# Optimization experiments

Measured on AMD Instinct MI355X. Metric: run time of the kernel, lower is better.

## Reference

```python
import jax, jax.numpy as jnp
import numpy as np

B, N_N, N_A, D = 1024, 96, 96, 512


def _normalize(x):
    return x / jnp.linalg.norm(x, axis=-1, keepdims=True)


def setup_inputs() -> dict:
    key = jax.random.key(0)
    ks = jax.random.split(key, 8)
    img_embs = _normalize(jax.random.normal(ks[0], (B, D), jnp.float32))
    normal_text_embs = _normalize(jax.random.normal(ks[1], (N_N, D), jnp.float32))
    abnormal_text_embs = _normalize(jax.random.normal(ks[2], (N_A, D), jnp.float32))
    logit_scale = jnp.full((1,), np.log(100.0), jnp.float32)  # CLIP temperature
    W1 = jax.random.normal(ks[3], (2 * D, D), jnp.float32) / np.sqrt(2 * D)
    b1 = jnp.zeros((D,), jnp.float32)
    W2 = jax.random.normal(ks[4], (D, D // 2), jnp.float32) / np.sqrt(D)
    b2 = jnp.zeros((D // 2,), jnp.float32)
    W3 = jax.random.normal(ks[5], (D // 2, D // 4), jnp.float32) / np.sqrt(D // 2)
    b3 = jnp.zeros((D // 4,), jnp.float32)
    return {"img_embs": img_embs, "normal_text_embs": normal_text_embs,
            "abnormal_text_embs": abnormal_text_embs, "logit_scale": logit_scale,
            "W1": W1, "b1": b1, "W2": W2, "b2": b2, "W3": W3, "b3": b3}


def _mlp(x, W1, b1, W2, b2, W3, b3):
    h = jax.nn.relu(x @ W1 + b1)
    h = jax.nn.relu(h @ W2 + b2)
    return h @ W3 + b3


def _branch(img_embs, text_embs, scale, W1, b1, W2, b2, W3, b3):
    # sims: [B, N]; softmax weights then exp-scaled text embeddings
    sims = (img_embs @ text_embs.T) * scale
    w = jax.nn.softmax(sims, axis=-1)
    scaled_text = text_embs[None, :, :] * jnp.exp(w)[:, :, None]      # [B, N, D]
    rep_img = jnp.broadcast_to(img_embs[:, None, :], scaled_text.shape)  # [B, N, D]
    x = jnp.concatenate([rep_img, scaled_text], axis=-1)              # [B, N, 2D]
    h = _mlp(x, W1, b1, W2, b2, W3, b3)                               # [B, N, D//4]
    return h.mean(axis=1)                                             # [B, D//4]


def reference(img_embs, normal_text_embs, abnormal_text_embs, logit_scale,
              W1, b1, W2, b2, W3, b3):
    scale = jnp.exp(logit_scale[0])
    h_n = _branch(img_embs, normal_text_embs, scale, W1, b1, W2, b2, W3, b3)
    h_a = _branch(img_embs, abnormal_text_embs, scale, W1, b1, W2, b2, W3, b3)
    return (h_n, h_a)
```

## Files before the change

### kernel.cpp

```cpp
#include <hip/hip_runtime.h>
#include <hip/hip_bf16.h>


typedef __attribute__((ext_vector_type(8))) short short8;
typedef __attribute__((ext_vector_type(4))) float floatx4;
typedef __attribute__((ext_vector_type(2))) float float2v;
typedef __attribute__((ext_vector_type(4))) unsigned int uint4v;

__device__ __forceinline__ unsigned short f2bf(float x) {
    unsigned int u = __float_as_uint(x);
    u += 0x7fffu + ((u >> 16) & 1u);
    return (unsigned short)(u >> 16);
}

template <bool BF16OUT>
__device__ __forceinline__ void gemm32(
    const float* __restrict__ A0, const float* __restrict__ A1, int rows0,
    const float* __restrict__ Bm, float* __restrict__ Cf,
    unsigned short* __restrict__ Cb, int mt, int nt, float* sAT, int t) {
    int r0 = mt * 32, c0 = nt * 64;
    int rg = t >> 4, cg = t & 15;
    int lrow = t >> 3, k4 = (t & 7) * 4;
    int gr = r0 + lrow;
    const float* Ap = (gr < rows0) ? (A0 + gr * 512) : (A1 + (gr - rows0) * 512);
    float acc[2][4];
#pragma unroll
    for (int r = 0; r < 2; r++)
#pragma unroll
        for (int c = 0; c < 4; c++) acc[r][c] = 0.f;
    const float* Bp = Bm + c0 + cg * 4;
    for (int k0 = 0; k0 < 512; k0 += 32) {
        __syncthreads();
        float4 av = *(const float4*)(Ap + k0 + k4);
        sAT[(k4 + 0) * 34 + lrow] = av.x;
        sAT[(k4 + 1) * 34 + lrow] = av.y;
        sAT[(k4 + 2) * 34 + lrow] = av.z;
        sAT[(k4 + 3) * 34 + lrow] = av.w;
        __syncthreads();
#pragma unroll 8
        for (int kk = 0; kk < 32; kk++) {
            float a0 = sAT[kk * 34 + rg * 2];
            float a1 = sAT[kk * 34 + rg * 2 + 1];
            float4 bv = *(const float4*)(Bp + (k0 + kk) * 512);
            acc[0][0] = fmaf(a0, bv.x, acc[0][0]); acc[0][1] = fmaf(a0, bv.y, acc[0][1]);
            acc[0][2] = fmaf(a0, bv.z, acc[0][2]); acc[0][3] = fmaf(a0, bv.w, acc[0][3]);
            acc[1][0] = fmaf(a1, bv.x, acc[1][0]); acc[1][1] = fmaf(a1, bv.y, acc[1][1]);
            acc[1][2] = fmaf(a1, bv.z, acc[1][2]); acc[1][3] = fmaf(a1, bv.w, acc[1][3]);
        }
    }
    int rr = r0 + rg * 2, cc = c0 + cg * 4;
#pragma unroll
    for (int r = 0; r < 2; r++) {
        if (BF16OUT) {
            unsigned long long pk =
                (unsigned long long)f2bf(acc[r][0]) | ((unsigned long long)f2bf(acc[r][1]) << 16) |
                ((unsigned long long)f2bf(acc[r][2]) << 32) | ((unsigned long long)f2bf(acc[r][3]) << 48);
            *(unsigned long long*)(Cb + (rr + r) * 512 + cc) = pk;
        } else {
            *(float4*)(Cf + (rr + r) * 512 + cc) = make_float4(acc[r][0], acc[r][1], acc[r][2], acc[r][3]);
        }
    }
}

__global__ __launch_bounds__(256) void prep_kernel(
    const float* __restrict__ img, const float* __restrict__ tn,
    const float* __restrict__ ta, const float* __restrict__ ls,
    const float* __restrict__ W1, const float* __restrict__ W2,
    float* __restrict__ e_ws, float* __restrict__ U_ws,
    unsigned short* __restrict__ Tb, unsigned short* __restrict__ W2Tf) {
    __shared__ __align__(16) float smem[8704];
    int idx = blockIdx.x;
    int t = threadIdx.x;

    if (idx < 256) {
        int bi0 = idx * 4;
        float* sImg = smem;
        float* sS   = smem + 2064;
        float* sMx  = smem + 2832;
        float* sSum = smem + 2840;
#pragma unroll
        for (int p = 0; p < 2; p++) {
            int i4 = t + 256 * p;
            int i = i4 >> 7, k4 = (i4 & 127) * 4;
            float4 v = *(const float4*)(img + (bi0 + i) * 512 + k4);
            sImg[i * 516 + k4 + 0] = v.x; sImg[i * 516 + k4 + 1] = v.y;
            sImg[i * 516 + k4 + 2] = v.z; sImg[i * 516 + k4 + 3] = v.w;
        }
        __syncthreads();
        float scale = __expf(ls[0]);
        int i = t & 3, n0 = (t >> 2) * 3;
        const float* txp[3];
#pragma unroll
        for (int r = 0; r < 3; r++) {
            int n = n0 + r;
            txp[r] = (n < 96) ? (tn + n * 512) : (ta + (n - 96) * 512);
        }
        float d0 = 0.f, d1 = 0.f, d2 = 0.f;
        const float* ib = &sImg[i * 516];
#pragma unroll 4
        for (int k4 = 0; k4 < 512; k4 += 4) {
            float4 iv = *(const float4*)(ib + k4);
            float4 a = *(const float4*)(txp[0] + k4);
            float4 b = *(const float4*)(txp[1] + k4);
            float4 c = *(const float4*)(txp[2] + k4);
            d0 += iv.x * a.x + iv.y * a.y + iv.z * a.z + iv.w * a.w;
            d1 += iv.x * b.x + iv.y * b.y + iv.z * b.z + iv.w * b.w;
            d2 += iv.x * c.x + iv.y * c.y + iv.z * c.z + iv.w * c.w;
        }
        sS[i * 192 + n0 + 0] = d0 * scale;
        sS[i * 192 + n0 + 1] = d1 * scale;
        sS[i * 192 + n0 + 2] = d2 * scale;
        __syncthreads();
        if (t < 8) {
            int ii = t >> 1, brx = t & 1;
            const float* base = &sS[ii * 192 + brx * 96];
            float m = -1e30f;
            for (int n = 0; n < 96; n++) m = fmaxf(m, base[n]);
            float s = 0.f;
            for (int n = 0; n < 96; n++) s += __expf(base[n] - m);
            sMx[t] = m; sSum[t] = s;
        }
        __syncthreads();
#pragma unroll
        for (int p = 0; p < 3; p++) {
            int j = t + 256 * p;
            int ii = j & 3, n = j >> 2;
            int brx = (n >= 96) ? 1 : 0;
            int nn = n - brx * 96;
            float w = __expf(sS[ii * 192 + n] - sMx[ii * 2 + brx]) / sSum[ii * 2 + brx];
            e_ws[(brx * 1024 + bi0 + ii) * 96 + nn] = __expf(w);
        }
    } else if (idx < 512) {
        int i2 = idx - 256;
        gemm32<false>(img, img, 1 << 20, W1, U_ws, nullptr, i2 >> 3, i2 & 7, smem, t);
    } else if (idx < 560) {
        int i2 = idx - 512;
        gemm32<true>(tn, ta, 96, W1 + 512 * 512, nullptr, Tb, i2 >> 3, i2 & 7, smem, t);
    } else {
        int kt = idx - 560;
        int k0 = kt * 32;
        float* sWT = smem;
        int kr = t >> 3, n0 = (t & 7) * 32;
#pragma unroll
        for (int c = 0; c < 8; c++) {
            float4 v = *(const float4*)(W2 + (k0 + kr) * 256 + n0 + c * 4);
            sWT[(n0 + c * 4 + 0) * 33 + kr] = v.x;
            sWT[(n0 + c * 4 + 1) * 33 + kr] = v.y;
            sWT[(n0 + c * 4 + 2) * 33 + kr] = v.z;
            sWT[(n0 + c * 4 + 3) * 33 + kr] = v.w;
        }
        __syncthreads();
        int lane = t & 63;
        int kl = (lane >> 4) * 8;
#pragma unroll
        for (int it = 0; it < 4; it++) {
            int nt = it * 4 + (t >> 6);
            int n = nt * 16 + (lane & 15);
            uint4v u;
#pragma unroll
            for (int c = 0; c < 4; c++) {
                unsigned short lo = f2bf(sWT[n * 33 + kl + 2 * c]);
                unsigned short hi = f2bf(sWT[n * 33 + kl + 2 * c + 1]);
                u[c] = (unsigned int)lo | ((unsigned int)hi << 16);
            }
            *(uint4v*)(W2Tf + (((kt * 16 + nt) * 64) + lane) * 8) = u;
        }
    }
}

__device__ __forceinline__ uint4v stage8(float ev, short8 tv, const float2v* u2) {
    uint4v tp; __builtin_memcpy(&tp, &tv, 16);
    float2v e2 = {ev, ev};
    const float2v z2 = {0.f, 0.f};
    uint4v pk;
#pragma unroll
    for (int jj = 0; jj < 4; jj++) {
        float2v t2;
        t2.x = __uint_as_float(tp[jj] << 16);
        t2.y = __uint_as_float(tp[jj] & 0xffff0000u);
        float2v f = __builtin_elementwise_fma(e2, t2, u2[jj]);
        f = __builtin_elementwise_max(f, z2);
        __hip_bfloat162 h2 = __float22bfloat162_rn(make_float2(f.x, f.y));
        unsigned int bits; __builtin_memcpy(&bits, &h2, 4);
        pk[jj] = bits;
    }
    return pk;
}

__global__ __launch_bounds__(256, 3) void branch_mlp9(
    const float* __restrict__ U, const unsigned short* __restrict__ Tb,
    const float* __restrict__ e_all, const unsigned short* __restrict__ W2Tf,
    const float* __restrict__ b1, const float* __restrict__ b2,
    const float* __restrict__ W3, const float* __restrict__ b3,
    float* __restrict__ out) {
    int b = blockIdx.x, br = blockIdx.y;
    const unsigned short* T = Tb + br * (96 * 512);

    __shared__ float sUb[512];
    __shared__ float sE[96];
    __shared__ __align__(16) unsigned short sH[2][96 * 64];
    __shared__ float sM2[256];
    __shared__ float sPart[256];

    int t = threadIdx.x;
    sUb[t] = U[b * 512 + t] + b1[t];
    sUb[t + 256] = U[b * 512 + t + 256] + b1[t + 256];
    if (t < 96) sE[t] = e_all[(br * 1024 + b) * 96 + t];

    const int wave = t >> 6, lane = t & 63;
    const int frow = lane & 15, fkq = (lane >> 4) * 8;
    const int f7 = frow & 7;
    const int srow = t >> 3;
    const int skc = (t & 7) * 8;
    const int sw = skc ^ ((srow & 7) * 8);
    const int ka0 = (((fkq >> 3) ^ f7) << 3);
    const int ka1 = (((4 + (fkq >> 3)) ^ f7) << 3);

    const floatx4 fz = {0.f, 0.f, 0.f, 0.f};
    floatx4 acc[6][4];
#pragma unroll
    for (int mt = 0; mt < 6; mt++)
#pragma unroll
        for (int j = 0; j < 4; j++) acc[mt][j] = fz;

    short8 tv[3];
#pragma unroll
    for (int i2 = 0; i2 < 3; i2++)
        tv[i2] = *(const short8*)(T + (srow + 32 * i2) * 512 + skc);
    const unsigned short* Wf = W2Tf + (wave * 4 * 64 + lane) * 8;

    __syncthreads();

    float ev[3];
#pragma unroll
    for (int i2 = 0; i2 < 3; i2++) ev[i2] = sE[srow + 32 * i2];

    {
        float2v u2[4];
#pragma unroll
        for (int jj = 0; jj < 4; jj++) u2[jj] = *(const float2v*)(&sUb[skc + 2 * jj]);
#pragma unroll
        for (int i2 = 0; i2 < 3; i2++)
            *(uint4v*)(&sH[0][(srow + 32 * i2) * 64 + sw]) = stage8(ev[i2], tv[i2], u2);
    }

#pragma unroll
    for (int s = 0; s < 8; s++) {
        int k0 = s * 64;
        unsigned short* sHb = sH[s & 1];
        __syncthreads();

        short8 b0f[4], b1f[4];
#pragma unroll
        for (int j = 0; j < 4; j++)
            b0f[j] = *(const short8*)(Wf + ((2 * s) * 16 + j) * (64 * 8));
#pragma unroll
        for (int j = 0; j < 4; j++)
            b1f[j] = *(const short8*)(Wf + ((2 * s + 1) * 16 + j) * (64 * 8));
        if (s < 7) {
#pragma unroll
            for (int i2 = 0; i2 < 3; i2++)
                tv[i2] = *(const short8*)(T + (srow + 32 * i2) * 512 + k0 + 64 + skc);
        }

#pragma unroll
        for (int mt = 0; mt < 6; mt++) {
            short8 afr = *(const short8*)(&sHb[(mt * 16 + frow) * 64 + ka0]);
#pragma unroll
            for (int j = 0; j < 4; j++)
                acc[mt][j] = __builtin_amdgcn_mfma_f32_16x16x32_bf16(afr, b0f[j], acc[mt][j], 0, 0, 0);
        }
#pragma unroll
        for (int mt = 0; mt < 6; mt++) {
            short8 afr = *(const short8*)(&sHb[(mt * 16 + frow) * 64 + ka1]);
#pragma unroll
            for (int j = 0; j < 4; j++)
                acc[mt][j] = __builtin_amdgcn_mfma_f32_16x16x32_bf16(afr, b1f[j], acc[mt][j], 0, 0, 0);
        }

        if (s < 7) {
            unsigned short* sHn = sH[(s + 1) & 1];
            float2v u2[4];
#pragma unroll
            for (int jj = 0; jj < 4; jj++) u2[jj] = *(const float2v*)(&sUb[k0 + 64 + skc + 2 * jj]);
#pragma unroll
            for (int i2 = 0; i2 < 3; i2++)
                *(uint4v*)(&sHn[(srow + 32 * i2) * 64 + sw]) = stage8(ev[i2], tv[i2], u2);
        }
    }

#pragma unroll
    for (int j = 0; j < 4; j++) {
        int col = wave * 64 + j * 16 + frow;
        float bb = b2[col];
        float s = 0.f;
#pragma unroll
        for (int mt = 0; mt < 6; mt++)
#pragma unroll
            for (int r = 0; r < 4; r++)
                s += fmaxf(acc[mt][j][r] + bb, 0.f);
        s += __shfl_xor(s, 16);
        s += __shfl_xor(s, 32);
        if (lane < 16) sM2[col] = s * (1.0f / 96.0f);
    }
    __syncthreads();

    int col = t & 127, ks2 = t >> 7;
    const float* w3p = W3 + (ks2 * 128) * 128 + col;
    const float* mp = sM2 + ks2 * 128;
    float o = 0.f;
#pragma unroll 8
    for (int k = 0; k < 128; k++) o = fmaf(mp[k], w3p[k * 128], o);
    sPart[t] = o;
    __syncthreads();
    if (t < 128) out[(br * 1024 + b) * 128 + t] = sPart[t] + sPart[t + 128] + b3[t];
}

extern "C" void kernel_launch(void* const* d_in, const int* in_sizes, int n_in,
                              void* d_out, int out_size, void* d_ws, size_t ws_size,
                              hipStream_t stream) {
    const float* img = (const float*)d_in[0];
    const float* tn  = (const float*)d_in[1];
    const float* ta  = (const float*)d_in[2];
    const float* ls  = (const float*)d_in[3];
    const float* W1  = (const float*)d_in[4];
    const float* b1  = (const float*)d_in[5];
    const float* W2  = (const float*)d_in[6];
    const float* b2  = (const float*)d_in[7];
    const float* W3  = (const float*)d_in[8];
    const float* b3  = (const float*)d_in[9];
    float* out = (float*)d_out;
    float* ws  = (float*)d_ws;

    float* e_ws = ws;
    float* U_ws = ws + 196608;
    unsigned short* Tb   = (unsigned short*)(ws + 720896);
    unsigned short* W2Tf = (unsigned short*)(ws + 770048);

    prep_kernel<<<576, 256, 0, stream>>>(img, tn, ta, ls, W1, W2, e_ws, U_ws, Tb, W2Tf);
    branch_mlp9<<<dim3(1024, 2), 256, 0, stream>>>(U_ws, Tb, e_ws, W2Tf, b1, b2, W3, b3, out);
}
```

Before: 177.5 us.

## Split branch MLP block across 8 waves to halve per-wave accumulators

Doubles the branch_mlp block to 512 threads, so each of 8 waves computes 32 output columns instead of 64, which halves the accumulator and B-fragment registers per wave. The staging work for the 96 rows is redistributed: the first 256 threads stage two rows and the rest stage one. The final W3 reduction is split four ways. The goal is more resident waves per CU to hide latency. In exchange, each A fragment is reused across fewer MFMAs, LDS reads per MFMA rise, and the staging load across threads is uneven.

New measurement: 177.5 us. About the same (+0.0%).

```diff
diff --git a/kernel.cpp b/kernel.cpp
--- a/kernel.cpp
+++ b/kernel.cpp
@@ -187,7 +187,7 @@
     return pk;
 }
 
-__global__ __launch_bounds__(256, 3) void branch_mlp9(
+__global__ __launch_bounds__(512, 4) void branch_mlp11(
     const float* __restrict__ U, const unsigned short* __restrict__ Tb,
     const float* __restrict__ e_all, const unsigned short* __restrict__ W2Tf,
     const float* __restrict__ b1, const float* __restrict__ b2,
@@ -200,48 +200,45 @@
     __shared__ float sE[96];
     __shared__ __align__(16) unsigned short sH[2][96 * 64];
     __shared__ float sM2[256];
-    __shared__ float sPart[256];
+    __shared__ float sPart[512];
 
     int t = threadIdx.x;
     sUb[t] = U[b * 512 + t] + b1[t];
-    sUb[t + 256] = U[b * 512 + t + 256] + b1[t + 256];
     if (t < 96) sE[t] = e_all[(br * 1024 + b) * 96 + t];
 
     const int wave = t >> 6, lane = t & 63;
     const int frow = lane & 15, fkq = (lane >> 4) * 8;
     const int f7 = frow & 7;
-    const int srow = t >> 3;
+    const bool two = (t < 256);
+    const int srowA = two ? (t >> 3) : (64 + ((t - 256) >> 3));
+    const int srowB = two ? (srowA + 32) : srowA;
     const int skc = (t & 7) * 8;
-    const int sw = skc ^ ((srow & 7) * 8);
+    const int sw = skc ^ ((srowA & 7) * 8);
     const int ka0 = (((fkq >> 3) ^ f7) << 3);
     const int ka1 = (((4 + (fkq >> 3)) ^ f7) << 3);
 
     const floatx4 fz = {0.f, 0.f, 0.f, 0.f};
-    floatx4 acc[6][4];
-#pragma unroll
-    for (int mt = 0; mt < 6; mt++)
-#pragma unroll
-        for (int j = 0; j < 4; j++) acc[mt][j] = fz;
-
-    short8 tv[3];
-#pragma unroll
-    for (int i2 = 0; i2 < 3; i2++)
-        tv[i2] = *(const short8*)(T + (srow + 32 * i2) * 512 + skc);
-    const unsigned short* Wf = W2Tf + (wave * 4 * 64 + lane) * 8;
+    floatx4 acc[6][2];
+#pragma unroll
+    for (int mt = 0; mt < 6; mt++) {
+        acc[mt][0] = fz; acc[mt][1] = fz;
+    }
+
+    short8 tvA = *(const short8*)(T + srowA * 512 + skc);
+    short8 tvB = *(const short8*)(T + srowB * 512 + skc);
+    const unsigned short* Wf = W2Tf + (wave * 2 * 64 + lane) * 8;
 
     __syncthreads();
 
-    float ev[3];
-#pragma unroll
-    for (int i2 = 0; i2 < 3; i2++) ev[i2] = sE[srow + 32 * i2];
+    float evA = sE[srowA];
+    float evB = sE[srowB];
 
     {
         float2v u2[4];
 #pragma unroll
         for (int jj = 0; jj < 4; jj++) u2[jj] = *(const float2v*)(&sUb[skc + 2 * jj]);
-#pragma unroll
-        for (int i2 = 0; i2 < 3; i2++)
-            *(uint4v*)(&sH[0][(srow + 32 * i2) * 64 + sw]) = stage8(ev[i2], tv[i2], u2);
+        *(uint4v*)(&sH[0][srowA * 64 + sw]) = stage8(evA, tvA, u2);
+        if (two) *(uint4v*)(&sH[0][srowB * 64 + sw]) = stage8(evB, tvB, u2);
     }
 
 #pragma unroll
@@ -250,48 +247,45 @@
         unsigned short* sHb = sH[s & 1];
         __syncthreads();
 
-        short8 b0f[4], b1f[4];
-#pragma unroll
-        for (int j = 0; j < 4; j++)
-            b0f[j] = *(const short8*)(Wf + ((2 * s) * 16 + j) * (64 * 8));
-#pragma unroll
-        for (int j = 0; j < 4; j++)
-            b1f[j] = *(const short8*)(Wf + ((2 * s + 1) * 16 + j) * (64 * 8));
+        short8 b0f[2], b1f[2];
+#pragma unroll
+        for (int j = 0; j < 2; j++)
+            b0f[j] = *(const short8*)(Wf + ((2 * s) * 16 + j) * 512);
+#pragma unroll
+        for (int j = 0; j < 2; j++)
+            b1f[j] = *(const short8*)(Wf + ((2 * s + 1) * 16 + j) * 512);
         if (s < 7) {
-#pragma unroll
-            for (int i2 = 0; i2 < 3; i2++)
-                tv[i2] = *(const short8*)(T + (srow + 32 * i2) * 512 + k0 + 64 + skc);
+            tvA = *(const short8*)(T + srowA * 512 + k0 + 64 + skc);
+            tvB = *(const short8*)(T + srowB * 512 + k0 + 64 + skc);
         }
 
 #pragma unroll
         for (int mt = 0; mt < 6; mt++) {
             short8 afr = *(const short8*)(&sHb[(mt * 16 + frow) * 64 + ka0]);
-#pragma unroll
-            for (int j = 0; j < 4; j++)
-                acc[mt][j] = __builtin_amdgcn_mfma_f32_16x16x32_bf16(afr, b0f[j], acc[mt][j], 0, 0, 0);
+            acc[mt][0] = __builtin_amdgcn_mfma_f32_16x16x32_bf16(afr, b0f[0], acc[mt][0], 0, 0, 0);
+            acc[mt][1] = __builtin_amdgcn_mfma_f32_16x16x32_bf16(afr, b0f[1], acc[mt][1], 0, 0, 0);
         }
 #pragma unroll
         for (int mt = 0; mt < 6; mt++) {
             short8 afr = *(const short8*)(&sHb[(mt * 16 + frow) * 64 + ka1]);
-#pragma unroll
-            for (int j = 0; j < 4; j++)
-                acc[mt][j] = __builtin_amdgcn_mfma_f32_16x16x32_bf16(afr, b1f[j], acc[mt][j], 0, 0, 0);
+            acc[mt][0] = __builtin_amdgcn_mfma_f32_16x16x32_bf16(afr, b1f[0], acc[mt][0], 0, 0, 0);
+            acc[mt][1] = __builtin_amdgcn_mfma_f32_16x16x32_bf16(afr, b1f[1], acc[mt][1], 0, 0, 0);
         }
 
         if (s < 7) {
             unsigned short* sHn = sH[(s + 1) & 1];
             float2v u2[4];
 #pragma unroll
-            for (int jj = 0; jj < 4; jj++) u2[jj] = *(const float2v*)(&sUb[k0 + 64 + skc + 2 * jj]);
-#pragma unroll
-            for (int i2 = 0; i2 < 3; i2++)
-                *(uint4v*)(&sHn[(srow + 32 * i2) * 64 + sw]) = stage8(ev[i2], tv[i2], u2);
-        }
-    }
-
-#pragma unroll
-    for (int j = 0; j < 4; j++) {
-        int col = wave * 64 + j * 16 + frow;
+            for (int jj = 0; jj < 4; jj++)
+                u2[jj] = *(const float2v*)(&sUb[k0 + 64 + skc + 2 * jj]);
+            *(uint4v*)(&sHn[srowA * 64 + sw]) = stage8(evA, tvA, u2);
+            if (two) *(uint4v*)(&sHn[srowB * 64 + sw]) = stage8(evB, tvB, u2);
+        }
+    }
+
+#pragma unroll
+    for (int j = 0; j < 2; j++) {
+        int col = wave * 32 + j * 16 + frow;
         float bb = b2[col];
         float s = 0.f;
 #pragma unroll
@@ -305,15 +299,17 @@
     }
     __syncthreads();
 
-    int col = t & 127, ks2 = t >> 7;
-    const float* w3p = W3 + (ks2 * 128) * 128 + col;
-    const float* mp = sM2 + ks2 * 128;
+    int col = t & 127, kq = t >> 7;
+    const float* w3p = W3 + (kq * 64) * 128 + col;
+    const float* mp = sM2 + kq * 64;
     float o = 0.f;
 #pragma unroll 8
-    for (int k = 0; k < 128; k++) o = fmaf(mp[k], w3p[k * 128], o);
+    for (int k = 0; k < 64; k++) o = fmaf(mp[k], w3p[k * 128], o);
     sPart[t] = o;
     __syncthreads();
-    if (t < 128) out[(br * 1024 + b) * 128 + t] = sPart[t] + sPart[t + 128] + b3[t];
+    if (t < 128)
+        out[(br * 1024 + b) * 128 + t] =
+            sPart[t] + sPart[t + 128] + sPart[t + 256] + sPart[t + 384] + b3[t];
 }
 
 extern "C" void kernel_launch(void* const* d_in, const int* in_sizes, int n_in,
@@ -338,5 +334,5 @@
     unsigned short* W2Tf = (unsigned short*)(ws + 770048);
 
     prep_kernel<<<576, 256, 0, stream>>>(img, tn, ta, ls, W1, W2, e_ws, U_ws, Tb, W2Tf);
-    branch_mlp9<<<dim3(1024, 2), 256, 0, stream>>>(U_ws, Tb, e_ws, W2Tf, b1, b2, W3, b3, out);
-}
+    branch_mlp11<<<dim3(1024, 2), 512, 0, stream>>>(U_ws, Tb, e_ws, W2Tf, b1, b2, W3, b3, out);
+}
```
